# Performance work log

Measured on AMD Instinct MI355X. Metric: run time of the kernel, lower is better.

## Reference

```python
import jax, jax.numpy as jnp
import numpy as np
from jax import lax

VOCAB, EM, UNITS, B, T = 32000, 256, 512, 64, 16


def setup_inputs() -> dict:
    key = jax.random.key(0)
    ks = jax.random.split(key, 8)
    return {
        "inputs": jax.random.randint(ks[0], (B, T), 0, VOCAB),
        "enc_h": jax.random.normal(ks[1], (B, UNITS), jnp.float32),
        "enc_c": jax.random.normal(ks[2], (B, UNITS), jnp.float32),
        "emb_table": jax.random.normal(ks[3], (VOCAB, EM), jnp.float32) * 0.02,
        "Wx": jax.random.normal(ks[4], (EM, 4 * UNITS), jnp.float32) * 0.02,
        "Wh": jax.random.normal(ks[5], (UNITS, 4 * UNITS), jnp.float32) * 0.02,
        "b": jnp.zeros((4 * UNITS,), jnp.float32),
        "Wout": jax.random.normal(ks[6], (T * UNITS, VOCAB), jnp.float32) * 0.02,
        "bout": jnp.zeros((VOCAB,), jnp.float32),
    }


def reference(inputs, enc_h, enc_c, emb_table, Wx, Wh, b, Wout, bout):
    # Embedding lookup: [B,T,EM]. mask_zero=False -> no mask.
    em = emb_table[inputs]
    # Precompute input contribution to all gates: [T,B,4U]
    xz = (jnp.einsum('bte,eu->btu', em, Wx) + b).transpose(1, 0, 2)

    def step(carry, xz_t):
        h, c = carry
        z = xz_t + h @ Wh                     # [B,4U]
        i, f, g, o = jnp.split(z, 4, axis=-1)  # keras gate order i,f,c,o
        i = jax.nn.sigmoid(i)
        f = jax.nn.sigmoid(f)
        g = jax.nn.sigmoid(g)   # activation='sigmoid' (non-default)
        o = jax.nn.sigmoid(o)
        c = f * c + i * g
        h = o * jax.nn.sigmoid(c)  # activation='sigmoid' on cell output too
        return (h, c), h

    _, hs = lax.scan(step, (enc_h, enc_c), xz)   # hs: [T,B,U]
    flat = hs.transpose(1, 0, 2).reshape(B, T * UNITS)
    logits = flat @ Wout + bout
    return jax.nn.softmax(logits, axis=-1)
```

## Files before the change

kernel.cpp:

```cpp
#include <hip/hip_runtime.h>
#include <math.h>

#define VOCAB 32000
#define EM    256
#define UNITS 512
#define BATCH 64
#define TSTEP 16
#define G4    (4*UNITS)
#define KFLAT (TSTEP*UNITS)
#define KSPLIT 4

typedef __bf16 bf16x8 __attribute__((ext_vector_type(8)));
typedef float  f32x4  __attribute__((ext_vector_type(4)));
union FragU { unsigned short u[8]; bf16x8 v; };

__device__ __align__(16) float g_xz [TSTEP*BATCH*G4];
__device__ __align__(16) float g_ht0[UNITS*BATCH];
__device__ __align__(16) float g_ht1[UNITS*BATCH];
__device__ __align__(16) float g_c0 [BATCH*UNITS];
__device__ __align__(16) float g_c1 [BATCH*UNITS];
__device__ __align__(16) unsigned short g_Ah[BATCH*KFLAT];
__device__ __align__(16) unsigned short g_Al[BATCH*KFLAT];
__device__ __align__(16) float g_part[KSPLIT*BATCH*VOCAB];

__device__ __forceinline__ float sigmoidf_(float x) {
    return 1.0f / (1.0f + expf(-x));
}
__device__ __forceinline__ unsigned short f2bf(float f) {
    unsigned u = __float_as_uint(f);
    return (unsigned short)((u + 0x7fffu + ((u >> 16) & 1u)) >> 16);
}
__device__ __forceinline__ float bf2f(unsigned short h) {
    return __uint_as_float((unsigned)h << 16);
}

__global__ __launch_bounds__(256) void transpose_h_kernel(const float* __restrict__ src)
{
    int i = blockIdx.x * 256 + threadIdx.x;
    int b = i >> 9, u = i & 511;
    g_ht0[u*BATCH + b] = src[i];
}

__global__ __launch_bounds__(256) void xz_kernel(
    const int* __restrict__ inputs, const float* __restrict__ emb,
    const float* __restrict__ Wx, const float* __restrict__ bias)
{
    const int col = blockIdx.x * 256 + threadIdx.x;
    const int r0  = blockIdx.y * 4;
    const float* e[4];
    #pragma unroll
    for (int i = 0; i < 4; ++i) {
        int r = r0 + i, t = r >> 6, b = r & 63;
        e[i] = emb + (size_t)inputs[b*TSTEP + t]*EM;
    }
    float a0 = bias[col], a1 = a0, a2 = a0, a3 = a0;
    #pragma unroll 4
    for (int k = 0; k < EM; ++k) {
        float w = Wx[(size_t)k*G4 + col];
        a0 = fmaf(e[0][k], w, a0);
        a1 = fmaf(e[1][k], w, a1);
        a2 = fmaf(e[2][k], w, a2);
        a3 = fmaf(e[3][k], w, a3);
    }
    g_xz[(size_t)(r0+0)*G4 + col] = a0;
    g_xz[(size_t)(r0+1)*G4 + col] = a1;
    g_xz[(size_t)(r0+2)*G4 + col] = a2;
    g_xz[(size_t)(r0+3)*G4 + col] = a3;
}

__global__ __launch_bounds__(256) void lstm_step_kernel(
    const float* __restrict__ Wh, const float* __restrict__ enc_c, int t)
{
    const float* h_in  = (t & 1) ? g_ht1 : g_ht0;
    float*       h_out = (t & 1) ? g_ht0 : g_ht1;
    const float* c_in  = (t == 0) ? enc_c : ((t & 1) ? g_c0 : g_c1);
    float*       c_out = (t & 1) ? g_c1 : g_c0;

    __shared__ float zp[2][128][4];
    const int tid  = threadIdx.x;
    const int ci   = tid & 127, kh = tid >> 7;
    const int gate = ci >> 5, ul = ci & 31;
    const int u0   = blockIdx.x * 32;
    const int b0   = blockIdx.y * 4;
    const int col  = gate*UNITS + u0 + ul;

    float a0, a1, a2, a3;
    if (kh == 0) {
        const float* xz = g_xz + ((size_t)t*BATCH + b0)*G4 + col;
        a0 = xz[0]; a1 = xz[G4]; a2 = xz[2*G4]; a3 = xz[3*G4];
    } else {
        a0 = a1 = a2 = a3 = 0.f;
    }
    const int k0 = kh * 256;
    #pragma unroll 4
    for (int k = k0; k < k0 + 256; ++k) {
        float w = Wh[(size_t)k*G4 + col];
        const float4 hv = *reinterpret_cast<const float4*>(h_in + (size_t)k*BATCH + b0);
        a0 = fmaf(hv.x, w, a0);
        a1 = fmaf(hv.y, w, a1);
        a2 = fmaf(hv.z, w, a2);
        a3 = fmaf(hv.w, w, a3);
    }
    zp[kh][ci][0] = a0; zp[kh][ci][1] = a1;
    zp[kh][ci][2] = a2; zp[kh][ci][3] = a3;
    __syncthreads();

    if (tid < 128) {
        const int bl = tid >> 5, u2 = tid & 31;
        const int b = b0 + bl, u = u0 + u2;
        float zi = zp[0][0*32 + u2][bl] + zp[1][0*32 + u2][bl];
        float zf = zp[0][1*32 + u2][bl] + zp[1][1*32 + u2][bl];
        float zg = zp[0][2*32 + u2][bl] + zp[1][2*32 + u2][bl];
        float zo = zp[0][3*32 + u2][bl] + zp[1][3*32 + u2][bl];
        float c = sigmoidf_(zf) * c_in[(size_t)b*UNITS + u] + sigmoidf_(zi) * sigmoidf_(zg);
        float h = sigmoidf_(zo) * sigmoidf_(c);
        c_out[(size_t)b*UNITS + u] = c;
        h_out[(size_t)u*BATCH + b] = h;
        unsigned short hh = f2bf(h);
        size_t ai = (size_t)b*KFLAT + t*UNITS + u;
        g_Ah[ai] = hh;
        g_Al[ai] = f2bf(h - bf2f(hh));
    }
}

__global__ __launch_bounds__(256, 4) void logits_mfma_kernel(
    const float* __restrict__ Wout)
{
    const int tid = threadIdx.x;
    const int wv  = tid >> 6, l = tid & 63;
    const int r   = l & 15, g = l >> 4;
    const int g8  = g * 8;
    const int n0  = blockIdx.x * 128 + wv * 32;
    const int k0  = blockIdx.y * (KFLAT / KSPLIT);

    f32x4 acc[4][2];
    #pragma unroll
    for (int ms = 0; ms < 4; ++ms)
        #pragma unroll
        for (int nt = 0; nt < 2; ++nt)
            acc[ms][nt] = (f32x4){0.f, 0.f, 0.f, 0.f};

    for (int kk = 0; kk < KFLAT / KSPLIT; kk += 32) {
        const int kbase = k0 + kk + g8;
        FragU ah[4], al[4];
        #pragma unroll
        for (int ms = 0; ms < 4; ++ms) {
            size_t aoff = (size_t)(ms*16 + r)*KFLAT + kbase;
            ah[ms].v = *reinterpret_cast<const bf16x8*>(g_Ah + aoff);
            al[ms].v = *reinterpret_cast<const bf16x8*>(g_Al + aoff);
        }
        #pragma unroll
        for (int nt = 0; nt < 2; ++nt) {
            const float* wB = Wout + (size_t)kbase * VOCAB + n0 + nt*16 + r;
            float w[8];
            #pragma unroll
            for (int j = 0; j < 8; ++j)
                w[j] = __builtin_nontemporal_load(wB + (size_t)j * VOCAB);
            FragU bh, bl;
            #pragma unroll
            for (int j = 0; j < 8; ++j) {
                unsigned short hi = f2bf(w[j]);
                bh.u[j] = hi;
                bl.u[j] = f2bf(w[j] - bf2f(hi));
            }
            #pragma unroll
            for (int ms = 0; ms < 4; ++ms)
                acc[ms][nt] = __builtin_amdgcn_mfma_f32_16x16x32_bf16(ah[ms].v, bh.v, acc[ms][nt], 0, 0, 0);
            #pragma unroll
            for (int ms = 0; ms < 4; ++ms)
                acc[ms][nt] = __builtin_amdgcn_mfma_f32_16x16x32_bf16(al[ms].v, bh.v, acc[ms][nt], 0, 0, 0);
            #pragma unroll
            for (int ms = 0; ms < 4; ++ms)
                acc[ms][nt] = __builtin_amdgcn_mfma_f32_16x16x32_bf16(ah[ms].v, bl.v, acc[ms][nt], 0, 0, 0);
        }
    }
    float* pp = g_part + (size_t)blockIdx.y * BATCH * VOCAB;
    #pragma unroll
    for (int ms = 0; ms < 4; ++ms) {
        #pragma unroll
        for (int nt = 0; nt < 2; ++nt) {
            #pragma unroll
            for (int j = 0; j < 4; ++j) {
                int m = ms*16 + g*4 + j;
                pp[(size_t)m*VOCAB + n0 + nt*16 + r] = acc[ms][nt][j];
            }
        }
    }
}

__global__ __launch_bounds__(1024) void combine_softmax_kernel(
    const float* __restrict__ bout, float* __restrict__ out)
{
    const int m = blockIdx.x;
    const int tid = threadIdx.x;
    const int wid = tid >> 6, lane = tid & 63;
    __shared__ float red[16];
    float* po = out + (size_t)m * VOCAB;

    float mx = -3.0e38f;
    for (int n = tid; n < VOCAB; n += 1024) {
        float v = g_part[(size_t)0*BATCH*VOCAB + (size_t)m*VOCAB + n]
                + g_part[(size_t)1*BATCH*VOCAB + (size_t)m*VOCAB + n]
                + g_part[(size_t)2*BATCH*VOCAB + (size_t)m*VOCAB + n]
                + g_part[(size_t)3*BATCH*VOCAB + (size_t)m*VOCAB + n]
                + bout[n];
        po[n] = v;
        mx = fmaxf(mx, v);
    }
    #pragma unroll
    for (int o = 32; o; o >>= 1) mx = fmaxf(mx, __shfl_xor(mx, o));
    if (lane == 0) red[wid] = mx;
    __syncthreads();
    mx = red[0];
    #pragma unroll
    for (int i = 1; i < 16; ++i) mx = fmaxf(mx, red[i]);
    __syncthreads();

    float s = 0.f;
    for (int n = tid; n < VOCAB; n += 1024) {
        float e = expf(po[n] - mx);
        po[n] = e;
        s += e;
    }
    #pragma unroll
    for (int o = 32; o; o >>= 1) s += __shfl_xor(s, o);
    if (lane == 0) red[wid] = s;
    __syncthreads();
    s = 0.f;
    #pragma unroll
    for (int i = 0; i < 16; ++i) s += red[i];
    float inv = 1.0f / s;

    for (int n = tid; n < VOCAB; n += 1024) po[n] *= inv;
}

extern "C" void kernel_launch(void* const* d_in, const int* in_sizes, int n_in,
                              void* d_out, int out_size, void* d_ws, size_t ws_size,
                              hipStream_t stream) {
    const int*   inputs = (const int*)  d_in[0];
    const float* enc_h  = (const float*)d_in[1];
    const float* enc_c  = (const float*)d_in[2];
    const float* emb    = (const float*)d_in[3];
    const float* Wx     = (const float*)d_in[4];
    const float* Wh     = (const float*)d_in[5];
    const float* bvec   = (const float*)d_in[6];
    const float* Wout   = (const float*)d_in[7];
    const float* bout   = (const float*)d_in[8];
    float* out = (float*)d_out;
    (void)d_ws; (void)ws_size; (void)in_sizes; (void)n_in; (void)out_size;

    transpose_h_kernel<<<128, 256, 0, stream>>>(enc_h);
    xz_kernel<<<dim3(8, 256), 256, 0, stream>>>(inputs, emb, Wx, bvec);

    for (int t = 0; t < TSTEP; ++t)
        lstm_step_kernel<<<dim3(16, 16), 256, 0, stream>>>(Wh, enc_c, t);

    logits_mfma_kernel<<<dim3(250, KSPLIT), 256, 0, stream>>>(Wout);
    combine_softmax_kernel<<<64, 1024, 0, stream>>>(bout, out);
}
```

Baseline: 881.4 us.

## Double-buffer logits GEMM loads, widen LSTM step grid, enlarge xz row tile

The logits MFMA kernel now software-pipelines its loop with two register buffers, issuing the next chunk's A fragments and Wout loads before the current chunk's MFMAs, and lowers the occupancy hint from 4 to 3 blocks to leave room for the extra registers. Its bf16 hi/lo split now uses native __bf16 casts. Each LSTM step kernel splits K four ways over 16 units per block, doubling the grid to 512 blocks for more parallelism on the latency-bound recurrence. The xz kernel computes 8 rows per thread instead of 4 to reuse each Wx load more. Together these target memory latency in the GEMM and underutilization in the small step kernels, at the cost of higher register pressure and a larger shared-memory reduction.

```diff
diff --git a/kernel.cpp b/kernel.cpp
--- a/kernel.cpp
+++ b/kernel.cpp
@@ -9,10 +9,11 @@
 #define G4    (4*UNITS)
 #define KFLAT (TSTEP*UNITS)
 #define KSPLIT 4
+#define KR    (KFLAT/KSPLIT)
 
 typedef __bf16 bf16x8 __attribute__((ext_vector_type(8)));
 typedef float  f32x4  __attribute__((ext_vector_type(4)));
-union FragU { unsigned short u[8]; bf16x8 v; };
+union FragU { __bf16 b[8]; bf16x8 v; };
 
 __device__ __align__(16) float g_xz [TSTEP*BATCH*G4];
 __device__ __align__(16) float g_ht0[UNITS*BATCH];
@@ -46,26 +47,26 @@
     const float* __restrict__ Wx, const float* __restrict__ bias)
 {
     const int col = blockIdx.x * 256 + threadIdx.x;
-    const int r0  = blockIdx.y * 4;
-    const float* e[4];
-    #pragma unroll
-    for (int i = 0; i < 4; ++i) {
+    const int r0  = blockIdx.y * 8;
+    const float* e[8];
+    #pragma unroll
+    for (int i = 0; i < 8; ++i) {
         int r = r0 + i, t = r >> 6, b = r & 63;
         e[i] = emb + (size_t)inputs[b*TSTEP + t]*EM;
     }
-    float a0 = bias[col], a1 = a0, a2 = a0, a3 = a0;
-    #pragma unroll 4
+    float a[8];
+    float bb = bias[col];
+    #pragma unroll
+    for (int i = 0; i < 8; ++i) a[i] = bb;
+    #pragma unroll 2
     for (int k = 0; k < EM; ++k) {
         float w = Wx[(size_t)k*G4 + col];
-        a0 = fmaf(e[0][k], w, a0);
-        a1 = fmaf(e[1][k], w, a1);
-        a2 = fmaf(e[2][k], w, a2);
-        a3 = fmaf(e[3][k], w, a3);
-    }
-    g_xz[(size_t)(r0+0)*G4 + col] = a0;
-    g_xz[(size_t)(r0+1)*G4 + col] = a1;
-    g_xz[(size_t)(r0+2)*G4 + col] = a2;
-    g_xz[(size_t)(r0+3)*G4 + col] = a3;
+        #pragma unroll
+        for (int i = 0; i < 8; ++i) a[i] = fmaf(e[i][k], w, a[i]);
+    }
+    #pragma unroll
+    for (int i = 0; i < 8; ++i)
+        g_xz[(size_t)(r0+i)*G4 + col] = a[i];
 }
 
 __global__ __launch_bounds__(256) void lstm_step_kernel(
@@ -76,11 +77,11 @@
     const float* c_in  = (t == 0) ? enc_c : ((t & 1) ? g_c0 : g_c1);
     float*       c_out = (t & 1) ? g_c1 : g_c0;
 
-    __shared__ float zp[2][128][4];
+    __shared__ float zp[4][64][4];
     const int tid  = threadIdx.x;
-    const int ci   = tid & 127, kh = tid >> 7;
-    const int gate = ci >> 5, ul = ci & 31;
-    const int u0   = blockIdx.x * 32;
+    const int ci   = tid & 63, kh = tid >> 6;
+    const int gate = ci >> 4, ul = ci & 15;
+    const int u0   = blockIdx.x * 16;
     const int b0   = blockIdx.y * 4;
     const int col  = gate*UNITS + u0 + ul;
 
@@ -91,9 +92,9 @@
     } else {
         a0 = a1 = a2 = a3 = 0.f;
     }
-    const int k0 = kh * 256;
+    const int k0 = kh * 128;
     #pragma unroll 4
-    for (int k = k0; k < k0 + 256; ++k) {
+    for (int k = k0; k < k0 + 128; ++k) {
         float w = Wh[(size_t)k*G4 + col];
         const float4 hv = *reinterpret_cast<const float4*>(h_in + (size_t)k*BATCH + b0);
         a0 = fmaf(hv.x, w, a0);
@@ -105,13 +106,13 @@
     zp[kh][ci][2] = a2; zp[kh][ci][3] = a3;
     __syncthreads();
 
-    if (tid < 128) {
-        const int bl = tid >> 5, u2 = tid & 31;
+    if (tid < 64) {
+        const int bl = tid >> 4, u2 = tid & 15;
         const int b = b0 + bl, u = u0 + u2;
-        float zi = zp[0][0*32 + u2][bl] + zp[1][0*32 + u2][bl];
-        float zf = zp[0][1*32 + u2][bl] + zp[1][1*32 + u2][bl];
-        float zg = zp[0][2*32 + u2][bl] + zp[1][2*32 + u2][bl];
-        float zo = zp[0][3*32 + u2][bl] + zp[1][3*32 + u2][bl];
+        float zi = zp[0][0*16+u2][bl] + zp[1][0*16+u2][bl] + zp[2][0*16+u2][bl] + zp[3][0*16+u2][bl];
+        float zf = zp[0][1*16+u2][bl] + zp[1][1*16+u2][bl] + zp[2][1*16+u2][bl] + zp[3][1*16+u2][bl];
+        float zg = zp[0][2*16+u2][bl] + zp[1][2*16+u2][bl] + zp[2][2*16+u2][bl] + zp[3][2*16+u2][bl];
+        float zo = zp[0][3*16+u2][bl] + zp[1][3*16+u2][bl] + zp[2][3*16+u2][bl] + zp[3][3*16+u2][bl];
         float c = sigmoidf_(zf) * c_in[(size_t)b*UNITS + u] + sigmoidf_(zi) * sigmoidf_(zg);
         float h = sigmoidf_(zo) * sigmoidf_(c);
         c_out[(size_t)b*UNITS + u] = c;
@@ -123,7 +124,51 @@
     }
 }
 
-__global__ __launch_bounds__(256, 4) void logits_mfma_kernel(
+__device__ __forceinline__ void load_chunk(
+    int kb, int r, int n0, const float* __restrict__ Wout,
+    FragU ah[4], FragU al[4], float wB[2][8])
+{
+    #pragma unroll
+    for (int ms = 0; ms < 4; ++ms) {
+        size_t aoff = (size_t)(ms*16 + r)*KFLAT + kb;
+        ah[ms].v = *reinterpret_cast<const bf16x8*>(g_Ah + aoff);
+        al[ms].v = *reinterpret_cast<const bf16x8*>(g_Al + aoff);
+    }
+    #pragma unroll
+    for (int nt = 0; nt < 2; ++nt) {
+        const float* wp = Wout + (size_t)kb * VOCAB + n0 + nt*16 + r;
+        #pragma unroll
+        for (int j = 0; j < 8; ++j)
+            wB[nt][j] = __builtin_nontemporal_load(wp + (size_t)j * VOCAB);
+    }
+}
+
+__device__ __forceinline__ void compute_chunk(
+    FragU ah[4], FragU al[4], float wB[2][8], f32x4 acc[4][2])
+{
+    #pragma unroll
+    for (int nt = 0; nt < 2; ++nt) {
+        FragU bh, bl;
+        #pragma unroll
+        for (int j = 0; j < 8; ++j) {
+            float w = wB[nt][j];
+            __bf16 hi = (__bf16)w;
+            bh.b[j] = hi;
+            bl.b[j] = (__bf16)(w - (float)hi);
+        }
+        #pragma unroll
+        for (int ms = 0; ms < 4; ++ms)
+            acc[ms][nt] = __builtin_amdgcn_mfma_f32_16x16x32_bf16(ah[ms].v, bh.v, acc[ms][nt], 0, 0, 0);
+        #pragma unroll
+        for (int ms = 0; ms < 4; ++ms)
+            acc[ms][nt] = __builtin_amdgcn_mfma_f32_16x16x32_bf16(al[ms].v, bh.v, acc[ms][nt], 0, 0, 0);
+        #pragma unroll
+        for (int ms = 0; ms < 4; ++ms)
+            acc[ms][nt] = __builtin_amdgcn_mfma_f32_16x16x32_bf16(ah[ms].v, bl.v, acc[ms][nt], 0, 0, 0);
+    }
+}
+
+__global__ __launch_bounds__(256, 3) void logits_mfma_kernel(
     const float* __restrict__ Wout)
 {
     const int tid = threadIdx.x;
@@ -131,7 +176,7 @@
     const int r   = l & 15, g = l >> 4;
     const int g8  = g * 8;
     const int n0  = blockIdx.x * 128 + wv * 32;
-    const int k0  = blockIdx.y * (KFLAT / KSPLIT);
+    const int k0  = blockIdx.y * KR;
 
     f32x4 acc[4][2];
     #pragma unroll
@@ -140,40 +185,19 @@
         for (int nt = 0; nt < 2; ++nt)
             acc[ms][nt] = (f32x4){0.f, 0.f, 0.f, 0.f};
 
-    for (int kk = 0; kk < KFLAT / KSPLIT; kk += 32) {
-        const int kbase = k0 + kk + g8;
-        FragU ah[4], al[4];
-        #pragma unroll
-        for (int ms = 0; ms < 4; ++ms) {
-            size_t aoff = (size_t)(ms*16 + r)*KFLAT + kbase;
-            ah[ms].v = *reinterpret_cast<const bf16x8*>(g_Ah + aoff);
-            al[ms].v = *reinterpret_cast<const bf16x8*>(g_Al + aoff);
-        }
-        #pragma unroll
-        for (int nt = 0; nt < 2; ++nt) {
-            const float* wB = Wout + (size_t)kbase * VOCAB + n0 + nt*16 + r;
-            float w[8];
-            #pragma unroll
-            for (int j = 0; j < 8; ++j)
-                w[j] = __builtin_nontemporal_load(wB + (size_t)j * VOCAB);
-            FragU bh, bl;
-            #pragma unroll
-            for (int j = 0; j < 8; ++j) {
-                unsigned short hi = f2bf(w[j]);
-                bh.u[j] = hi;
-                bl.u[j] = f2bf(w[j] - bf2f(hi));
-            }
-            #pragma unroll
-            for (int ms = 0; ms < 4; ++ms)
-                acc[ms][nt] = __builtin_amdgcn_mfma_f32_16x16x32_bf16(ah[ms].v, bh.v, acc[ms][nt], 0, 0, 0);
-            #pragma unroll
-            for (int ms = 0; ms < 4; ++ms)
-                acc[ms][nt] = __builtin_amdgcn_mfma_f32_16x16x32_bf16(al[ms].v, bh.v, acc[ms][nt], 0, 0, 0);
-            #pragma unroll
-            for (int ms = 0; ms < 4; ++ms)
-                acc[ms][nt] = __builtin_amdgcn_mfma_f32_16x16x32_bf16(ah[ms].v, bl.v, acc[ms][nt], 0, 0, 0);
-        }
-    }
+    FragU ahA[4], alA[4]; float wA[2][8];
+    FragU ahB[4], alB[4]; float wB_[2][8];
+
+    load_chunk(k0 + g8, r, n0, Wout, ahA, alA, wA);
+    for (int c = 0; c < 64; c += 2) {
+        int c1 = (c+1 < 64) ? c+1 : 63;
+        load_chunk(k0 + c1*32 + g8, r, n0, Wout, ahB, alB, wB_);
+        compute_chunk(ahA, alA, wA, acc);
+        int c2 = (c+2 < 64) ? c+2 : 63;
+        load_chunk(k0 + c2*32 + g8, r, n0, Wout, ahA, alA, wA);
+        compute_chunk(ahB, alB, wB_, acc);
+    }
+
     float* pp = g_part + (size_t)blockIdx.y * BATCH * VOCAB;
     #pragma unroll
     for (int ms = 0; ms < 4; ++ms) {
@@ -250,10 +274,10 @@
     (void)d_ws; (void)ws_size; (void)in_sizes; (void)n_in; (void)out_size;
 
     transpose_h_kernel<<<128, 256, 0, stream>>>(enc_h);
-    xz_kernel<<<dim3(8, 256), 256, 0, stream>>>(inputs, emb, Wx, bvec);
+    xz_kernel<<<dim3(8, 128), 256, 0, stream>>>(inputs, emb, Wx, bvec);
 
     for (int t = 0; t < TSTEP; ++t)
-        lstm_step_kernel<<<dim3(16, 16), 256, 0, stream>>>(Wh, enc_c, t);
+        lstm_step_kernel<<<dim3(32, 16), 256, 0, stream>>>(Wh, enc_c, t);
 
     logits_mfma_kernel<<<dim3(250, KSPLIT), 256, 0, stream>>>(Wout);
     combine_softmax_kernel<<<64, 1024, 0, stream>>>(bout, out);
```

After: 846.6 us. 4.0% less time.
